# Performance work log

Hardware: AMD Instinct MI355X
Metric: run time of the kernel (lower is better)

## Reference

```python
import jax, jax.numpy as jnp
import numpy as np

D_MODEL = 1024
N_HEADS = 16
D_K = D_MODEL // N_HEADS


def setup_inputs() -> dict:
    key = jax.random.key(0)
    ks = jax.random.split(key, 11)
    B, S = 2, 2048
    scale = 0.02
    inp = {
        "q": jax.random.normal(ks[0], (B, S, D_MODEL), jnp.float32),
        "k": jax.random.normal(ks[1], (B, S, D_MODEL), jnp.float32),
        "v": jax.random.normal(ks[2], (B, S, D_MODEL), jnp.float32),
        "w_q": jax.random.normal(ks[3], (D_MODEL, D_MODEL), jnp.float32) * scale,
        "b_q": jnp.zeros((D_MODEL,), jnp.float32),
        "w_k": jax.random.normal(ks[4], (D_MODEL, D_MODEL), jnp.float32) * scale,
        "b_k": jnp.zeros((D_MODEL,), jnp.float32),
        "w_v": jax.random.normal(ks[5], (D_MODEL, D_MODEL), jnp.float32) * scale,
        "b_v": jnp.zeros((D_MODEL,), jnp.float32),
        "w_o": jax.random.normal(ks[6], (D_MODEL, D_MODEL), jnp.float32) * scale,
        "b_o": jnp.zeros((D_MODEL,), jnp.float32),
    }
    return inp


def reference(q, k, v, w_q, b_q, w_k, b_k, w_v, b_v, w_o, b_o):
    B, S, _ = q.shape
    # projections (torch Linear: x @ W.T + b); split into heads -> [B, H, S, d]
    def proj(x, w, b):
        return (x @ w.T + b).reshape(B, S, N_HEADS, D_K).transpose(0, 2, 1, 3)
    qh = proj(q, w_q, b_q)
    kh = proj(k, w_k, b_k)
    vh = proj(v, w_v, b_v)
    scores = jnp.einsum("bhqd,bhkd->bhqk", qh, kh) / jnp.sqrt(
        jnp.asarray(D_K, jnp.float32))
    attn = jax.nn.softmax(scores, axis=-1)  # dropout = identity (eval)
    out = jnp.einsum("bhqk,bhkd->bhqd", attn, vh)
    out = out.transpose(0, 2, 1, 3).reshape(B, S, D_MODEL)
    return out @ w_o.T + b_o
```

## Files before the change

kernel.cpp:

```cpp
#include <hip/hip_runtime.h>

typedef unsigned short u16;
typedef unsigned int u32;
typedef __attribute__((ext_vector_type(4))) unsigned short u16x4;
typedef __attribute__((ext_vector_type(8))) unsigned short u16x8;
typedef __attribute__((ext_vector_type(8))) __bf16 bf16x8;
typedef __attribute__((ext_vector_type(4))) float f32x4;
typedef __attribute__((ext_vector_type(16))) float f32x16;

#define SEQ 2048
#define DMODEL 1024
#define LDP 3072
#define MM (DMODEL * DMODEL)
#define SC 0.18033688f

__device__ __forceinline__ u16 f2bf(float f) {
  unsigned u = __builtin_bit_cast(unsigned, f);
  u = (u + 0x7fffu + ((u >> 16) & 1u)) >> 16;
  return (u16)u;
}

__device__ __forceinline__ u32 cvtpk(float lo, float hi) {
  u32 r;
  asm volatile("v_cvt_pk_bf16_f32 %0, %1, %2" : "=v"(r) : "v"(lo), "v"(hi));
  return r;
}

__device__ __forceinline__ float fexp2(float x) {
#if __has_builtin(__builtin_amdgcn_exp2f)
  return __builtin_amdgcn_exp2f(x);
#else
  return exp2f(x);
#endif
}

__device__ __forceinline__ bf16x8 ldbf8(const u16* p) {
  return __builtin_bit_cast(bf16x8, *(const u16x8*)p);
}
__device__ __forceinline__ bf16x8 ldbf8c(const char* p) {
  return __builtin_bit_cast(bf16x8, *(const u16x8*)p);
}

__device__ __forceinline__ f32x4 mfma16(bf16x8 a, bf16x8 b, f32x4 c) {
  return __builtin_amdgcn_mfma_f32_16x16x32_bf16(a, b, c, 0, 0, 0);
}
__device__ __forceinline__ f32x16 mfma32(bf16x8 a, bf16x8 b, f32x16 c) {
  return __builtin_amdgcn_mfma_f32_32x32x16_bf16(a, b, c, 0, 0, 0);
}

__device__ __forceinline__ void gl16(const void* g, void* l) {
  __builtin_amdgcn_global_load_lds(
      (__attribute__((address_space(1))) void*)(size_t)g,
      (__attribute__((address_space(3))) void*)l, 16, 0, 0);
}

__device__ __forceinline__ void cast8(const float* __restrict__ s, u16* __restrict__ d) {
  const size_t i = ((size_t)blockIdx.x * blockDim.x + threadIdx.x) * 8;
  const float4 a = *(const float4*)(s + i);
  const float4 b = *(const float4*)(s + i + 4);
  u16x8 o;
  o[0] = f2bf(a.x); o[1] = f2bf(a.y); o[2] = f2bf(a.z); o[3] = f2bf(a.w);
  o[4] = f2bf(b.x); o[5] = f2bf(b.y); o[6] = f2bf(b.z); o[7] = f2bf(b.w);
  *(u16x8*)(d + i) = o;
}

__global__ void cast_qkv_k(const float* __restrict__ q, const float* __restrict__ k,
                           const float* __restrict__ v, u16* __restrict__ dq,
                           u16* __restrict__ dk, u16* __restrict__ dv) {
  const int z = blockIdx.y;
  cast8(z == 0 ? q : z == 1 ? k : v, z == 0 ? dq : z == 1 ? dk : dv);
}

__global__ void cast_w_k(const float* __restrict__ wq, const float* __restrict__ wk,
                         const float* __restrict__ wv, const float* __restrict__ wo,
                         u16* __restrict__ wqkv, u16* __restrict__ wob) {
  const int z = blockIdx.y;
  const float* s = z == 0 ? wq : z == 1 ? wk : z == 2 ? wv : wo;
  u16* d = z < 3 ? wqkv + (size_t)z * MM : wob;
  cast8(s, d);
}

template <int OMODE>
__device__ __forceinline__ void gemm_bt_body(const u16* __restrict__ A,
                                             const u16* __restrict__ Bw,
                                             const float* __restrict__ bias,
                                             void* __restrict__ Cv, const int K,
                                             const int ldc, const int ncol0,
                                             const int m0, const int n0) {
  __shared__ u16 As[128 * 32];
  __shared__ u16 Bs[128 * 32];
  const int tid = threadIdx.x;
  const int lane = tid & 63;
  const int w = tid >> 6;
  const int l15 = lane & 15;
  const int lg = lane >> 4;

  f32x4 acc[4][4] = {};

  const int arow = (w >> 1) * 64 + l15;
  const int brow = (w & 1) * 64 + l15;
  const int kfb = lg * 16;

  const int strow = w * 32 + (lane >> 2);
  const u16* Ag = A + (size_t)(m0 + strow) * K + (lane & 3) * 8;
  const u16* Bg = Bw + (size_t)(n0 + strow) * K + (lane & 3) * 8;
  const size_t rstep = (size_t)16 * K;
  char* AsL0 = (char*)As + w * 32 * 64;
  char* AsL1 = AsL0 + 16 * 64;
  char* BsL0 = (char*)Bs + w * 32 * 64;
  char* BsL1 = BsL0 + 16 * 64;

  for (int k0 = 0; k0 < K; k0 += 32) {
    __syncthreads();
    gl16(Ag + k0, AsL0);
    gl16(Ag + k0 + rstep, AsL1);
    gl16(Bg + k0, BsL0);
    gl16(Bg + k0 + rstep, BsL1);
    __syncthreads();
    bf16x8 af[4], bfv[4];
#pragma unroll
    for (int t = 0; t < 4; ++t) {
      af[t] = ldbf8c((char*)As + (arow + t * 16) * 64 + kfb);
      bfv[t] = ldbf8c((char*)Bs + (brow + t * 16) * 64 + kfb);
    }
    __builtin_amdgcn_s_setprio(1);
#pragma unroll
    for (int i = 0; i < 4; ++i)
#pragma unroll
      for (int j = 0; j < 4; ++j) acc[i][j] = mfma16(af[i], bfv[j], acc[i][j]);
    __builtin_amdgcn_s_setprio(0);
  }

  const int mrow = (w >> 1) * 64 + lg * 4;
  const int ncol = (w & 1) * 64 + l15;
#pragma unroll
  for (int j = 0; j < 4; ++j) {
    const int gn = n0 + ncol + j * 16;
    const float bia = bias[gn];
#pragma unroll
    for (int i = 0; i < 4; ++i) {
      const int gmb = m0 + mrow + i * 16;
#pragma unroll
      for (int r = 0; r < 4; ++r) {
        const float val = acc[i][j][r] + bia;
        const int gm = gmb + r;
        if (OMODE == 0) {
          ((float*)Cv)[(size_t)gm * ldc + gn] = val;
        } else if (OMODE == 1) {
          ((u16*)Cv)[(size_t)gm * ldc + ncol0 + gn] = f2bf(val);
        } else {
          const int bb = gm >> 11, ss = gm & 2047;
          const int hh = gn >> 6, dd = gn & 63;
          ((u16*)Cv)[(((size_t)(bb * 16 + hh) * 64 + dd) << 11) + ss] = f2bf(val);
        }
      }
    }
  }
}

__global__ __launch_bounds__(256, 3) void gemm_qkv_k(
    const u16* __restrict__ qb, const u16* __restrict__ kb,
    const u16* __restrict__ vb, const u16* __restrict__ wqkv,
    const float* __restrict__ bq, const float* __restrict__ bk,
    const float* __restrict__ bv, u16* __restrict__ proj, u16* __restrict__ vtb) {
  const int b = blockIdx.x;
  const int xcd = b & 7;
  const int i = b >> 3;
  const int z = i >> 5;
  const int j = i & 31;
  const int m0 = (xcd * 4 + (j >> 3)) * 128;
  const int n0 = (j & 7) * 128;
  if (z == 2)
    gemm_bt_body<2>(vb, wqkv + 2 * (size_t)MM, bv, vtb, DMODEL, 0, 0, m0, n0);
  else
    gemm_bt_body<1>(z == 0 ? qb : kb, wqkv + (size_t)z * MM, z == 0 ? bq : bk,
                    proj, DMODEL, LDP, z * DMODEL, m0, n0);
}

__global__ __launch_bounds__(256, 3) void gemm_o_k(const u16* __restrict__ attnb,
                                                   const u16* __restrict__ wob,
                                                   const float* __restrict__ bo,
                                                   float* __restrict__ out) {
  const int b = blockIdx.x;
  const int xcd = b & 7;
  const int i = b >> 3;
  const int m0 = (xcd * 4 + (i >> 3)) * 128;
  const int n0 = (i & 7) * 128;
  gemm_bt_body<0>(attnb, wob, bo, out, DMODEL, DMODEL, 0, m0, n0);
}

__global__ __launch_bounds__(256, 2) void attn_k(const u16* __restrict__ proj,
                                                 const u16* __restrict__ vtb,
                                                 u16* __restrict__ outa) {
  __shared__ u16 ks[2][64 * 64];
  __shared__ u16 vs[2][64 * 64];
  const int b = blockIdx.x;
  const int slot = b >> 3;
  const int bh = (b & 7) * 4 + (slot >> 4);
  const int qB = (slot & 15) * 128;
  const int tid = threadIdx.x;
  const int lane = tid & 63;
  const int w = tid >> 6;
  const size_t rb = (size_t)(bh >> 4) * SEQ;
  const int h = bh & 15;
  const int l31 = lane & 31;
  const int hi = lane >> 5;
  const int swz = (l31 & 7) << 4;

  const u16* qp = proj + (rb + qB + w * 32 + l31) * LDP + h * 64 + hi * 8;
  bf16x8 qf[4];
#pragma unroll
  for (int km = 0; km < 4; ++km) qf[km] = ldbf8(qp + km * 16);

  const int srow = tid >> 2;
  const int scel = (tid & 3) * 16;
  const int stz0 = srow * 128 + (((tid & 3) * 32) ^ ((srow & 7) << 4));
  const int stz1 = srow * 128 + ((((tid & 3) * 32) + 16) ^ ((srow & 7) << 4));
  const u16* kg = proj + rb * LDP + DMODEL + h * 64;
  const u16* vg = vtb + (size_t)bh * 64 * SEQ;

  u16x8 ka0, ka1, va0, va1;
  {
    const u16* kr = kg + (size_t)srow * LDP + scel;
    ka0 = *(const u16x8*)kr;
    ka1 = *(const u16x8*)(kr + 8);
    const u16* vr = vg + (size_t)srow * SEQ + scel;
    va0 = *(const u16x8*)vr;
    va1 = *(const u16x8*)(vr + 8);
  }

  f32x16 oa0 = {}, oa1 = {};
  float mrun = -3.0e38f, lrun = 0.f;
  int p = 0;

  for (int kv0 = 0; kv0 < SEQ; kv0 += 64) {
    {
      char* kd = (char*)ks[p];
      char* vd = (char*)vs[p];
      *(u16x8*)(kd + stz0) = ka0;
      *(u16x8*)(kd + stz1) = ka1;
      *(u16x8*)(vd + stz0) = va0;
      *(u16x8*)(vd + stz1) = va1;
    }
    __syncthreads();
    if (kv0 + 64 < SEQ) {
      const u16* kr = kg + (size_t)(kv0 + 64 + srow) * LDP + scel;
      ka0 = *(const u16x8*)kr;
      ka1 = *(const u16x8*)(kr + 8);
      const u16* vr = vg + (size_t)srow * SEQ + kv0 + 64 + scel;
      va0 = *(const u16x8*)vr;
      va1 = *(const u16x8*)(vr + 8);
    }
    const char* kp = (const char*)ks[p];
    const char* vp = (const char*)vs[p];
    f32x16 s0 = {}, s1 = {};
    __builtin_amdgcn_s_setprio(1);
#pragma unroll
    for (int km = 0; km < 4; ++km) {
      const int co = (km * 32 + hi * 16) ^ swz;
      const bf16x8 k0 = ldbf8c(kp + l31 * 128 + co);
      const bf16x8 k1 = ldbf8c(kp + (32 + l31) * 128 + co);
      s0 = mfma32(k0, qf[km], s0);
      s1 = mfma32(k1, qf[km], s1);
    }
    __builtin_amdgcn_s_setprio(0);

    float mxq0 = fmaxf(fmaxf(s0[0], s0[1]), fmaxf(s0[2], s0[3]));
    float mxq1 = fmaxf(fmaxf(s0[4], s0[5]), fmaxf(s0[6], s0[7]));
    float mxq2 = fmaxf(fmaxf(s0[8], s0[9]), fmaxf(s0[10], s0[11]));
    float mxq3 = fmaxf(fmaxf(s0[12], s0[13]), fmaxf(s0[14], s0[15]));
    float mxq4 = fmaxf(fmaxf(s1[0], s1[1]), fmaxf(s1[2], s1[3]));
    float mxq5 = fmaxf(fmaxf(s1[4], s1[5]), fmaxf(s1[6], s1[7]));
    float mxq6 = fmaxf(fmaxf(s1[8], s1[9]), fmaxf(s1[10], s1[11]));
    float mxq7 = fmaxf(fmaxf(s1[12], s1[13]), fmaxf(s1[14], s1[15]));
    float mx = fmaxf(fmaxf(fmaxf(mxq0, mxq1), fmaxf(mxq2, mxq3)),
                     fmaxf(fmaxf(mxq4, mxq5), fmaxf(mxq6, mxq7)));
    mx = fmaxf(mx, __shfl_xor(mx, 32));
    if (!__all(mx <= mrun + 64.0f)) {
      const float mn = fmaxf(mrun, mx);
      const float sf = fexp2((mrun - mn) * SC);
      mrun = mn;
      lrun *= sf;
#pragma unroll
      for (int r = 0; r < 16; ++r) { oa0[r] *= sf; oa1[r] *= sf; }
    }
    const float nmc = -mrun * SC;
#pragma unroll
    for (int r = 0; r < 16; ++r) s0[r] = fexp2(__builtin_fmaf(s0[r], SC, nmc));
#pragma unroll
    for (int r = 0; r < 16; ++r) s1[r] = fexp2(__builtin_fmaf(s1[r], SC, nmc));
    float rs = (((s0[0] + s0[1]) + (s0[2] + s0[3])) +
                ((s0[4] + s0[5]) + (s0[6] + s0[7]))) +
               (((s0[8] + s0[9]) + (s0[10] + s0[11])) +
                ((s0[12] + s0[13]) + (s0[14] + s0[15])));
    rs += (((s1[0] + s1[1]) + (s1[2] + s1[3])) +
           ((s1[4] + s1[5]) + (s1[6] + s1[7]))) +
          (((s1[8] + s1[9]) + (s1[10] + s1[11])) +
           ((s1[12] + s1[13]) + (s1[14] + s1[15])));
    rs += __shfl_xor(rs, 32);
    lrun += rs;

    __builtin_amdgcn_s_setprio(1);
#define PCHUNK(SV, G, CB)                                                \
    {                                                                    \
      u16x8 pbu;                                                         \
      ((u32*)&pbu)[0] = cvtpk(SV[G + 0], SV[G + 1]);                     \
      ((u32*)&pbu)[1] = cvtpk(SV[G + 2], SV[G + 3]);                     \
      ((u32*)&pbu)[2] = cvtpk(SV[G + 4], SV[G + 5]);                     \
      ((u32*)&pbu)[3] = cvtpk(SV[G + 6], SV[G + 7]);                     \
      const bf16x8 pb = __builtin_bit_cast(bf16x8, pbu);                 \
      const int vc0 = (CB + 8 * hi) ^ swz;                               \
      const int vc1 = (CB + 16 + 8 * hi) ^ swz;                          \
      const char* vr0 = vp + l31 * 128;                                  \
      const char* vr1 = vp + (32 + l31) * 128;                           \
      u16x8 vf0, vf1;                                                    \
      *(u16x4*)&vf0       = *(const u16x4*)(vr0 + vc0);                  \
      *((u16x4*)&vf0 + 1) = *(const u16x4*)(vr0 + vc1);                  \
      *(u16x4*)&vf1       = *(const u16x4*)(vr1 + vc0);                  \
      *((u16x4*)&vf1 + 1) = *(const u16x4*)(vr1 + vc1);                  \
      oa0 = mfma32(__builtin_bit_cast(bf16x8, vf0), pb, oa0);            \
      oa1 = mfma32(__builtin_bit_cast(bf16x8, vf1), pb, oa1);            \
    }
    PCHUNK(s0, 0, 0)
    PCHUNK(s0, 8, 32)
    PCHUNK(s1, 0, 64)
    PCHUNK(s1, 8, 96)
#undef PCHUNK
    __builtin_amdgcn_s_setprio(0);
    p ^= 1;
  }

  const float invl = 1.0f / lrun;
  u16* orow = outa + (rb + qB + w * 32 + l31) * DMODEL + h * 64 + hi * 4;
#pragma unroll
  for (int g = 0; g < 4; ++g) {
    u16x4 st0, st1;
    ((u32*)&st0)[0] = cvtpk(oa0[4 * g + 0] * invl, oa0[4 * g + 1] * invl);
    ((u32*)&st0)[1] = cvtpk(oa0[4 * g + 2] * invl, oa0[4 * g + 3] * invl);
    *(u16x4*)(orow + 8 * g) = st0;
    ((u32*)&st1)[0] = cvtpk(oa1[4 * g + 0] * invl, oa1[4 * g + 1] * invl);
    ((u32*)&st1)[1] = cvtpk(oa1[4 * g + 2] * invl, oa1[4 * g + 3] * invl);
    *(u16x4*)(orow + 32 + 8 * g) = st1;
  }
}

extern "C" void kernel_launch(void* const* d_in, const int* in_sizes, int n_in,
                              void* d_out, int out_size, void* d_ws, size_t ws_size,
                              hipStream_t stream) {
  const float* q  = (const float*)d_in[0];
  const float* k  = (const float*)d_in[1];
  const float* v  = (const float*)d_in[2];
  const float* wq = (const float*)d_in[3];
  const float* bq = (const float*)d_in[4];
  const float* wk = (const float*)d_in[5];
  const float* bk = (const float*)d_in[6];
  const float* wv = (const float*)d_in[7];
  const float* bv = (const float*)d_in[8];
  const float* wo = (const float*)d_in[9];
  const float* bo = (const float*)d_in[10];

  const size_t NTOK = (size_t)2 * SEQ;
  const size_t NELE = NTOK * DMODEL;
  u16* qb    = (u16*)d_ws;
  u16* kb    = qb + NELE;
  u16* vb    = kb + NELE;
  u16* wqkv  = vb + NELE;
  u16* wob   = wqkv + 3 * (size_t)MM;
  u16* projb = wob + (size_t)MM;
  u16* vtb   = projb + NTOK * LDP;
  u16* attnb = qb;

  cast_qkv_k<<<dim3(2048, 3), 256, 0, stream>>>(q, k, v, qb, kb, vb);
  cast_w_k<<<dim3(512, 4), 256, 0, stream>>>(wq, wk, wv, wo, wqkv, wob);
  gemm_qkv_k<<<768, 256, 0, stream>>>(qb, kb, vb, wqkv, bq, bk, bv, projb, vtb);
  attn_k<<<512, 256, 0, stream>>>(projb, vtb, attnb);
  gemm_o_k<<<256, 256, 0, stream>>>(attnb, wob, bo, (float*)d_out);
}
```

Before: 127.3 us.

## Process two KV tiles per attention iteration, retune V swizzle, merge cast kernels

The attention loop now handles 128 keys per iteration. Two 64-key K/V tiles sit in the two LDS buffers, so each iteration issues both QK^T products before running softmax and PV on each tile. This halves the number of barrier-separated iterations and gives more independent MFMA work to hide latency. The price is more registers for prefetch (8 vectors) and scores, and two barriers per iteration with no LDS overlap while writing. V now uses a separate 8-byte-granularity XOR swizzle meant to cut LDS bank conflicts on its 4-element reads. The two fp32-to-bf16 cast launches are merged into one kernel to save a launch.

Result: no change. 128.4 us (+0.8%).

```diff
diff --git a/kernel.cpp b/kernel.cpp
--- a/kernel.cpp
+++ b/kernel.cpp
@@ -54,30 +54,33 @@
       (__attribute__((address_space(3))) void*)l, 16, 0, 0);
 }
 
-__device__ __forceinline__ void cast8(const float* __restrict__ s, u16* __restrict__ d) {
-  const size_t i = ((size_t)blockIdx.x * blockDim.x + threadIdx.x) * 8;
+__global__ void cast_all_k(const float* __restrict__ q, const float* __restrict__ k,
+                           const float* __restrict__ v, const float* __restrict__ wq,
+                           const float* __restrict__ wk, const float* __restrict__ wv,
+                           const float* __restrict__ wo, u16* __restrict__ dq,
+                           u16* __restrict__ dk, u16* __restrict__ dv,
+                           u16* __restrict__ wqkv, u16* __restrict__ wob) {
+  int b = blockIdx.x;
+  const float* s;
+  u16* d;
+  if (b < 6144) {
+    const int z = b >> 11;
+    s = z == 0 ? q : z == 1 ? k : v;
+    d = z == 0 ? dq : z == 1 ? dk : dv;
+    b &= 2047;
+  } else {
+    const int z = (b - 6144) >> 9;
+    s = z == 0 ? wq : z == 1 ? wk : z == 2 ? wv : wo;
+    d = z < 3 ? wqkv + (size_t)z * MM : wob;
+    b = (b - 6144) & 511;
+  }
+  const size_t i = ((size_t)b * blockDim.x + threadIdx.x) * 8;
   const float4 a = *(const float4*)(s + i);
-  const float4 b = *(const float4*)(s + i + 4);
+  const float4 c = *(const float4*)(s + i + 4);
   u16x8 o;
   o[0] = f2bf(a.x); o[1] = f2bf(a.y); o[2] = f2bf(a.z); o[3] = f2bf(a.w);
-  o[4] = f2bf(b.x); o[5] = f2bf(b.y); o[6] = f2bf(b.z); o[7] = f2bf(b.w);
+  o[4] = f2bf(c.x); o[5] = f2bf(c.y); o[6] = f2bf(c.z); o[7] = f2bf(c.w);
   *(u16x8*)(d + i) = o;
-}
-
-__global__ void cast_qkv_k(const float* __restrict__ q, const float* __restrict__ k,
-                           const float* __restrict__ v, u16* __restrict__ dq,
-                           u16* __restrict__ dk, u16* __restrict__ dv) {
-  const int z = blockIdx.y;
-  cast8(z == 0 ? q : z == 1 ? k : v, z == 0 ? dq : z == 1 ? dk : dv);
-}
-
-__global__ void cast_w_k(const float* __restrict__ wq, const float* __restrict__ wk,
-                         const float* __restrict__ wv, const float* __restrict__ wo,
-                         u16* __restrict__ wqkv, u16* __restrict__ wob) {
-  const int z = blockIdx.y;
-  const float* s = z == 0 ? wq : z == 1 ? wk : z == 2 ? wv : wo;
-  u16* d = z < 3 ? wqkv + (size_t)z * MM : wob;
-  cast8(s, d);
 }
 
 template <int OMODE>
@@ -205,7 +208,8 @@
   const int h = bh & 15;
   const int l31 = lane & 31;
   const int hi = lane >> 5;
-  const int swz = (l31 & 7) << 4;
+  const int swzk = (l31 & 7) << 4;
+  const int swzv = (l31 & 15) << 3;
 
   const u16* qp = proj + (rb + qB + w * 32 + l31) * LDP + h * 64 + hi * 8;
   bf16x8 qf[4];
@@ -213,122 +217,159 @@
   for (int km = 0; km < 4; ++km) qf[km] = ldbf8(qp + km * 16);
 
   const int srow = tid >> 2;
-  const int scel = (tid & 3) * 16;
-  const int stz0 = srow * 128 + (((tid & 3) * 32) ^ ((srow & 7) << 4));
-  const int stz1 = srow * 128 + ((((tid & 3) * 32) + 16) ^ ((srow & 7) << 4));
+  const int scol = (tid & 3) * 32;
+  const int scel = scol >> 1;
+  const int kz0 = srow * 128 + (scol ^ ((srow & 7) << 4));
+  const int kz1 = srow * 128 + ((scol + 16) ^ ((srow & 7) << 4));
+  const int vz0 = srow * 128 + (scol ^ ((srow & 15) << 3));
+  const int vz1 = srow * 128 + ((scol + 8) ^ ((srow & 15) << 3));
+  const int vz2 = srow * 128 + ((scol + 16) ^ ((srow & 15) << 3));
+  const int vz3 = srow * 128 + ((scol + 24) ^ ((srow & 15) << 3));
   const u16* kg = proj + rb * LDP + DMODEL + h * 64;
   const u16* vg = vtb + (size_t)bh * 64 * SEQ;
 
-  u16x8 ka0, ka1, va0, va1;
-  {
-    const u16* kr = kg + (size_t)srow * LDP + scel;
-    ka0 = *(const u16x8*)kr;
-    ka1 = *(const u16x8*)(kr + 8);
-    const u16* vr = vg + (size_t)srow * SEQ + scel;
-    va0 = *(const u16x8*)vr;
-    va1 = *(const u16x8*)(vr + 8);
+  u16x8 kA0, kA1, kB0, kB1, vA0, vA1, vB0, vB1;
+
+#define LOADPAIR(KV)                                                     \
+  {                                                                      \
+    const u16* krA = kg + (size_t)((KV) + srow) * LDP + scel;            \
+    kA0 = *(const u16x8*)krA;                                            \
+    kA1 = *(const u16x8*)(krA + 8);                                      \
+    const u16* krB = kg + (size_t)((KV) + 64 + srow) * LDP + scel;       \
+    kB0 = *(const u16x8*)krB;                                            \
+    kB1 = *(const u16x8*)(krB + 8);                                      \
+    const u16* vrA = vg + (size_t)srow * SEQ + (KV) + scel;              \
+    vA0 = *(const u16x8*)vrA;                                            \
+    vA1 = *(const u16x8*)(vrA + 8);                                      \
+    vB0 = *(const u16x8*)(vrA + 64);                                     \
+    vB1 = *(const u16x8*)(vrA + 72);                                     \
+  }
+
+#define WRITEPAIR()                                                      \
+  {                                                                      \
+    char* k0d = (char*)ks[0];                                            \
+    char* k1d = (char*)ks[1];                                            \
+    char* v0d = (char*)vs[0];                                            \
+    char* v1d = (char*)vs[1];                                            \
+    *(u16x8*)(k0d + kz0) = kA0;                                          \
+    *(u16x8*)(k0d + kz1) = kA1;                                          \
+    *(u16x8*)(k1d + kz0) = kB0;                                          \
+    *(u16x8*)(k1d + kz1) = kB1;                                          \
+    *(u16x4*)(v0d + vz0) = *(u16x4*)&vA0;                                \
+    *(u16x4*)(v0d + vz1) = *((u16x4*)&vA0 + 1);                          \
+    *(u16x4*)(v0d + vz2) = *(u16x4*)&vA1;                                \
+    *(u16x4*)(v0d + vz3) = *((u16x4*)&vA1 + 1);                          \
+    *(u16x4*)(v1d + vz0) = *(u16x4*)&vB0;                                \
+    *(u16x4*)(v1d + vz1) = *((u16x4*)&vB0 + 1);                          \
+    *(u16x4*)(v1d + vz2) = *(u16x4*)&vB1;                                \
+    *(u16x4*)(v1d + vz3) = *((u16x4*)&vB1 + 1);                          \
+  }
+
+#define QKT(S0, S1, KP)                                                  \
+  {                                                                      \
+    __builtin_amdgcn_s_setprio(1);                                       \
+    _Pragma("unroll") for (int km = 0; km < 4; ++km) {                   \
+      const int co = (km * 32 + hi * 16) ^ swzk;                         \
+      const bf16x8 k0 = ldbf8c((KP) + l31 * 128 + co);                   \
+      const bf16x8 k1 = ldbf8c((KP) + (32 + l31) * 128 + co);            \
+      S0 = mfma32(k0, qf[km], S0);                                       \
+      S1 = mfma32(k1, qf[km], S1);                                       \
+    }                                                                    \
+    __builtin_amdgcn_s_setprio(0);                                       \
+  }
+
+#define PCHUNK(SV, G, CB, VP)                                            \
+  {                                                                      \
+    u16x8 pbu;                                                           \
+    ((u32*)&pbu)[0] = cvtpk(SV[G + 0], SV[G + 1]);                       \
+    ((u32*)&pbu)[1] = cvtpk(SV[G + 2], SV[G + 3]);                       \
+    ((u32*)&pbu)[2] = cvtpk(SV[G + 4], SV[G + 5]);                       \
+    ((u32*)&pbu)[3] = cvtpk(SV[G + 6], SV[G + 7]);                       \
+    const bf16x8 pb = __builtin_bit_cast(bf16x8, pbu);                   \
+    const int vc0 = ((CB) + 8 * hi) ^ swzv;                              \
+    const int vc1 = ((CB) + 16 + 8 * hi) ^ swzv;                         \
+    const char* vr0 = (VP) + l31 * 128;                                  \
+    const char* vr1 = (VP) + (32 + l31) * 128;                           \
+    u16x8 vf0, vf1;                                                      \
+    *(u16x4*)&vf0 = *(const u16x4*)(vr0 + vc0);                          \
+    *((u16x4*)&vf0 + 1) = *(const u16x4*)(vr0 + vc1);                    \
+    *(u16x4*)&vf1 = *(const u16x4*)(vr1 + vc0);                          \
+    *((u16x4*)&vf1 + 1) = *(const u16x4*)(vr1 + vc1);                    \
+    oa0 = mfma32(__builtin_bit_cast(bf16x8, vf0), pb, oa0);              \
+    oa1 = mfma32(__builtin_bit_cast(bf16x8, vf1), pb, oa1);              \
+  }
+
+#define SOFTPV(S0, S1, VP)                                               \
+  {                                                                      \
+    float mxq0 = fmaxf(fmaxf(S0[0], S0[1]), fmaxf(S0[2], S0[3]));        \
+    float mxq1 = fmaxf(fmaxf(S0[4], S0[5]), fmaxf(S0[6], S0[7]));        \
+    float mxq2 = fmaxf(fmaxf(S0[8], S0[9]), fmaxf(S0[10], S0[11]));      \
+    float mxq3 = fmaxf(fmaxf(S0[12], S0[13]), fmaxf(S0[14], S0[15]));    \
+    float mxq4 = fmaxf(fmaxf(S1[0], S1[1]), fmaxf(S1[2], S1[3]));        \
+    float mxq5 = fmaxf(fmaxf(S1[4], S1[5]), fmaxf(S1[6], S1[7]));        \
+    float mxq6 = fmaxf(fmaxf(S1[8], S1[9]), fmaxf(S1[10], S1[11]));      \
+    float mxq7 = fmaxf(fmaxf(S1[12], S1[13]), fmaxf(S1[14], S1[15]));    \
+    float mx = fmaxf(fmaxf(fmaxf(mxq0, mxq1), fmaxf(mxq2, mxq3)),        \
+                     fmaxf(fmaxf(mxq4, mxq5), fmaxf(mxq6, mxq7)));       \
+    mx = fmaxf(mx, __shfl_xor(mx, 32));                                  \
+    if (!__all(mx <= mrun + 64.0f)) {                                    \
+      const float mn = fmaxf(mrun, mx);                                  \
+      const float sf = fexp2((mrun - mn) * SC);                          \
+      mrun = mn;                                                         \
+      lrun *= sf;                                                        \
+      _Pragma("unroll") for (int r = 0; r < 16; ++r) {                   \
+        oa0[r] *= sf;                                                    \
+        oa1[r] *= sf;                                                    \
+      }                                                                  \
+    }                                                                    \
+    const float nmc = -mrun * SC;                                        \
+    _Pragma("unroll") for (int r = 0; r < 16; ++r)                       \
+        S0[r] = fexp2(__builtin_fmaf(S0[r], SC, nmc));                   \
+    _Pragma("unroll") for (int r = 0; r < 16; ++r)                       \
+        S1[r] = fexp2(__builtin_fmaf(S1[r], SC, nmc));                   \
+    float rs = (((S0[0] + S0[1]) + (S0[2] + S0[3])) +                    \
+                ((S0[4] + S0[5]) + (S0[6] + S0[7]))) +                   \
+               (((S0[8] + S0[9]) + (S0[10] + S0[11])) +                  \
+                ((S0[12] + S0[13]) + (S0[14] + S0[15])));                \
+    rs += (((S1[0] + S1[1]) + (S1[2] + S1[3])) +                         \
+           ((S1[4] + S1[5]) + (S1[6] + S1[7]))) +                        \
+          (((S1[8] + S1[9]) + (S1[10] + S1[11])) +                       \
+           ((S1[12] + S1[13]) + (S1[14] + S1[15])));                     \
+    rs += __shfl_xor(rs, 32);                                            \
+    lrun += rs;                                                          \
+    __builtin_amdgcn_s_setprio(1);                                       \
+    PCHUNK(S0, 0, 0, VP)                                                 \
+    PCHUNK(S0, 8, 32, VP)                                                \
+    PCHUNK(S1, 0, 64, VP)                                                \
+    PCHUNK(S1, 8, 96, VP)                                                \
+    __builtin_amdgcn_s_setprio(0);                                       \
   }
 
   f32x16 oa0 = {}, oa1 = {};
   float mrun = -3.0e38f, lrun = 0.f;
-  int p = 0;
-
-  for (int kv0 = 0; kv0 < SEQ; kv0 += 64) {
-    {
-      char* kd = (char*)ks[p];
-      char* vd = (char*)vs[p];
-      *(u16x8*)(kd + stz0) = ka0;
-      *(u16x8*)(kd + stz1) = ka1;
-      *(u16x8*)(vd + stz0) = va0;
-      *(u16x8*)(vd + stz1) = va1;
+
+  LOADPAIR(0);
+  WRITEPAIR();
+  __syncthreads();
+
+  for (int it = 0; it < SEQ / 128; ++it) {
+    if (it + 1 < SEQ / 128) LOADPAIR((it + 1) * 128);
+    f32x16 s0A = {}, s1A = {}, s0B = {}, s1B = {};
+    QKT(s0A, s1A, (const char*)ks[0])
+    QKT(s0B, s1B, (const char*)ks[1])
+    SOFTPV(s0A, s1A, (const char*)vs[0])
+    SOFTPV(s0B, s1B, (const char*)vs[1])
+    if (it + 1 < SEQ / 128) {
+      __syncthreads();
+      WRITEPAIR();
+      __syncthreads();
     }
-    __syncthreads();
-    if (kv0 + 64 < SEQ) {
-      const u16* kr = kg + (size_t)(kv0 + 64 + srow) * LDP + scel;
-      ka0 = *(const u16x8*)kr;
-      ka1 = *(const u16x8*)(kr + 8);
-      const u16* vr = vg + (size_t)srow * SEQ + kv0 + 64 + scel;
-      va0 = *(const u16x8*)vr;
-      va1 = *(const u16x8*)(vr + 8);
-    }
-    const char* kp = (const char*)ks[p];
-    const char* vp = (const char*)vs[p];
-    f32x16 s0 = {}, s1 = {};
-    __builtin_amdgcn_s_setprio(1);
-#pragma unroll
-    for (int km = 0; km < 4; ++km) {
-      const int co = (km * 32 + hi * 16) ^ swz;
-      const bf16x8 k0 = ldbf8c(kp + l31 * 128 + co);
-      const bf16x8 k1 = ldbf8c(kp + (32 + l31) * 128 + co);
-      s0 = mfma32(k0, qf[km], s0);
-      s1 = mfma32(k1, qf[km], s1);
-    }
-    __builtin_amdgcn_s_setprio(0);
-
-    float mxq0 = fmaxf(fmaxf(s0[0], s0[1]), fmaxf(s0[2], s0[3]));
-    float mxq1 = fmaxf(fmaxf(s0[4], s0[5]), fmaxf(s0[6], s0[7]));
-    float mxq2 = fmaxf(fmaxf(s0[8], s0[9]), fmaxf(s0[10], s0[11]));
-    float mxq3 = fmaxf(fmaxf(s0[12], s0[13]), fmaxf(s0[14], s0[15]));
-    float mxq4 = fmaxf(fmaxf(s1[0], s1[1]), fmaxf(s1[2], s1[3]));
-    float mxq5 = fmaxf(fmaxf(s1[4], s1[5]), fmaxf(s1[6], s1[7]));
-    float mxq6 = fmaxf(fmaxf(s1[8], s1[9]), fmaxf(s1[10], s1[11]));
-    float mxq7 = fmaxf(fmaxf(s1[12], s1[13]), fmaxf(s1[14], s1[15]));
-    float mx = fmaxf(fmaxf(fmaxf(mxq0, mxq1), fmaxf(mxq2, mxq3)),
-                     fmaxf(fmaxf(mxq4, mxq5), fmaxf(mxq6, mxq7)));
-    mx = fmaxf(mx, __shfl_xor(mx, 32));
-    if (!__all(mx <= mrun + 64.0f)) {
-      const float mn = fmaxf(mrun, mx);
-      const float sf = fexp2((mrun - mn) * SC);
-      mrun = mn;
-      lrun *= sf;
-#pragma unroll
-      for (int r = 0; r < 16; ++r) { oa0[r] *= sf; oa1[r] *= sf; }
-    }
-    const float nmc = -mrun * SC;
-#pragma unroll
-    for (int r = 0; r < 16; ++r) s0[r] = fexp2(__builtin_fmaf(s0[r], SC, nmc));
-#pragma unroll
-    for (int r = 0; r < 16; ++r) s1[r] = fexp2(__builtin_fmaf(s1[r], SC, nmc));
-    float rs = (((s0[0] + s0[1]) + (s0[2] + s0[3])) +
-                ((s0[4] + s0[5]) + (s0[6] + s0[7]))) +
-               (((s0[8] + s0[9]) + (s0[10] + s0[11])) +
-                ((s0[12] + s0[13]) + (s0[14] + s0[15])));
-    rs += (((s1[0] + s1[1]) + (s1[2] + s1[3])) +
-           ((s1[4] + s1[5]) + (s1[6] + s1[7]))) +
-          (((s1[8] + s1[9]) + (s1[10] + s1[11])) +
-           ((s1[12] + s1[13]) + (s1[14] + s1[15])));
-    rs += __shfl_xor(rs, 32);
-    lrun += rs;
-
-    __builtin_amdgcn_s_setprio(1);
-#define PCHUNK(SV, G, CB)                                                \
-    {                                                                    \
-      u16x8 pbu;                                                         \
-      ((u32*)&pbu)[0] = cvtpk(SV[G + 0], SV[G + 1]);                     \
-      ((u32*)&pbu)[1] = cvtpk(SV[G + 2], SV[G + 3]);                     \
-      ((u32*)&pbu)[2] = cvtpk(SV[G + 4], SV[G + 5]);                     \
-      ((u32*)&pbu)[3] = cvtpk(SV[G + 6], SV[G + 7]);                     \
-      const bf16x8 pb = __builtin_bit_cast(bf16x8, pbu);                 \
-      const int vc0 = (CB + 8 * hi) ^ swz;                               \
-      const int vc1 = (CB + 16 + 8 * hi) ^ swz;                          \
-      const char* vr0 = vp + l31 * 128;                                  \
-      const char* vr1 = vp + (32 + l31) * 128;                           \
-      u16x8 vf0, vf1;                                                    \
-      *(u16x4*)&vf0       = *(const u16x4*)(vr0 + vc0);                  \
-      *((u16x4*)&vf0 + 1) = *(const u16x4*)(vr0 + vc1);                  \
-      *(u16x4*)&vf1       = *(const u16x4*)(vr1 + vc0);                  \
-      *((u16x4*)&vf1 + 1) = *(const u16x4*)(vr1 + vc1);                  \
-      oa0 = mfma32(__builtin_bit_cast(bf16x8, vf0), pb, oa0);            \
-      oa1 = mfma32(__builtin_bit_cast(bf16x8, vf1), pb, oa1);            \
-    }
-    PCHUNK(s0, 0, 0)
-    PCHUNK(s0, 8, 32)
-    PCHUNK(s1, 0, 64)
-    PCHUNK(s1, 8, 96)
+  }
+#undef LOADPAIR
+#undef WRITEPAIR
+#undef QKT
 #undef PCHUNK
-    __builtin_amdgcn_s_setprio(0);
-    p ^= 1;
-  }
+#undef SOFTPV
 
   const float invl = 1.0f / lrun;
   u16* orow = outa + (rb + qB + w * 32 + l31) * DMODEL + h * 64 + hi * 4;
@@ -370,8 +411,8 @@
   u16* vtb   = projb + NTOK * LDP;
   u16* attnb = qb;
 
-  cast_qkv_k<<<dim3(2048, 3), 256, 0, stream>>>(q, k, v, qb, kb, vb);
-  cast_w_k<<<dim3(512, 4), 256, 0, stream>>>(wq, wk, wv, wo, wqkv, wob);
+  cast_all_k<<<8192, 256, 0, stream>>>(q, k, v, wq, wk, wv, wo, qb, kb, vb,
+                                       wqkv, wob);
   gemm_qkv_k<<<768, 256, 0, stream>>>(qb, kb, vb, wqkv, bq, bk, bv, projb, vtb);
   attn_k<<<512, 256, 0, stream>>>(projb, vtb, attnb);
   gemm_o_k<<<256, 256, 0, stream>>>(attnb, wob, bo, (float*)d_out);
```

## Fuse fp32-to-bf16 casts into GEMM tile loads and reswizzle V LDS layout

Applied to the files above, without the earlier changes.

Removes the two standalone cast kernels and makes the projection GEMMs load fp32 activations and weights directly. They convert to bf16 in registers and store into LDS, using register prefetch of the next K tile in place of async global-to-LDS copies. This saves the extra bf16 round trip through global memory and two launches. The cost is that each GEMM block reads twice the bytes per tile and re-converts weights redundantly across blocks. The attention kernel also gets a separate finer-grained XOR swizzle for the V tile to reduce LDS bank conflicts on its 8-byte reads.

Result: faster. 120.1 us (-5.7%).

```diff
diff --git a/kernel.cpp b/kernel.cpp
--- a/kernel.cpp
+++ b/kernel.cpp
@@ -48,41 +48,18 @@
   return __builtin_amdgcn_mfma_f32_32x32x16_bf16(a, b, c, 0, 0, 0);
 }
 
-__device__ __forceinline__ void gl16(const void* g, void* l) {
-  __builtin_amdgcn_global_load_lds(
-      (__attribute__((address_space(1))) void*)(size_t)g,
-      (__attribute__((address_space(3))) void*)l, 16, 0, 0);
-}
-
-__device__ __forceinline__ void cast8(const float* __restrict__ s, u16* __restrict__ d) {
-  const size_t i = ((size_t)blockIdx.x * blockDim.x + threadIdx.x) * 8;
-  const float4 a = *(const float4*)(s + i);
-  const float4 b = *(const float4*)(s + i + 4);
-  u16x8 o;
-  o[0] = f2bf(a.x); o[1] = f2bf(a.y); o[2] = f2bf(a.z); o[3] = f2bf(a.w);
-  o[4] = f2bf(b.x); o[5] = f2bf(b.y); o[6] = f2bf(b.z); o[7] = f2bf(b.w);
-  *(u16x8*)(d + i) = o;
-}
-
-__global__ void cast_qkv_k(const float* __restrict__ q, const float* __restrict__ k,
-                           const float* __restrict__ v, u16* __restrict__ dq,
-                           u16* __restrict__ dk, u16* __restrict__ dv) {
-  const int z = blockIdx.y;
-  cast8(z == 0 ? q : z == 1 ? k : v, z == 0 ? dq : z == 1 ? dk : dv);
-}
-
-__global__ void cast_w_k(const float* __restrict__ wq, const float* __restrict__ wk,
-                         const float* __restrict__ wv, const float* __restrict__ wo,
-                         u16* __restrict__ wqkv, u16* __restrict__ wob) {
-  const int z = blockIdx.y;
-  const float* s = z == 0 ? wq : z == 1 ? wk : z == 2 ? wv : wo;
-  u16* d = z < 3 ? wqkv + (size_t)z * MM : wob;
-  cast8(s, d);
-}
-
-template <int OMODE>
-__device__ __forceinline__ void gemm_bt_body(const u16* __restrict__ A,
-                                             const u16* __restrict__ Bw,
+__device__ __forceinline__ u16x8 pk8(float4 x, float4 y) {
+  u16x8 r;
+  ((u32*)&r)[0] = cvtpk(x.x, x.y);
+  ((u32*)&r)[1] = cvtpk(x.z, x.w);
+  ((u32*)&r)[2] = cvtpk(y.x, y.y);
+  ((u32*)&r)[3] = cvtpk(y.z, y.w);
+  return r;
+}
+
+template <int OMODE, int AFP32>
+__device__ __forceinline__ void gemm_bt_body(const void* __restrict__ Av,
+                                             const float* __restrict__ Bw,
                                              const float* __restrict__ bias,
                                              void* __restrict__ Cv, const int K,
                                              const int ldc, const int ncol0,
@@ -101,22 +78,50 @@
   const int brow = (w & 1) * 64 + l15;
   const int kfb = lg * 16;
 
-  const int strow = w * 32 + (lane >> 2);
-  const u16* Ag = A + (size_t)(m0 + strow) * K + (lane & 3) * 8;
-  const u16* Bg = Bw + (size_t)(n0 + strow) * K + (lane & 3) * 8;
-  const size_t rstep = (size_t)16 * K;
-  char* AsL0 = (char*)As + w * 32 * 64;
-  char* AsL1 = AsL0 + 16 * 64;
-  char* BsL0 = (char*)Bs + w * 32 * 64;
-  char* BsL1 = BsL0 + 16 * 64;
-
+  const int srow = tid >> 2;
+  const int sc8 = (tid & 3) * 8;
+  const float* Agf = (const float*)Av + (size_t)(m0 + srow) * K + sc8;
+  const u16* Agh = (const u16*)Av + (size_t)(m0 + srow) * K + sc8;
+  const float* Bgf = Bw + (size_t)(n0 + srow) * K + sc8;
+  const size_t rstep = (size_t)64 * K;
+
+  float4 a00, a01, a10, a11, b00, b01, b10, b11;
+  u16x8 ah0, ah1;
+
+#define GLOADK(KO)                                                       \
+  {                                                                      \
+    if (AFP32) {                                                         \
+      a00 = *(const float4*)(Agf + (KO));                                \
+      a01 = *(const float4*)(Agf + (KO) + 4);                            \
+      a10 = *(const float4*)(Agf + (KO) + rstep);                        \
+      a11 = *(const float4*)(Agf + (KO) + rstep + 4);                    \
+    } else {                                                             \
+      ah0 = *(const u16x8*)(Agh + (KO));                                 \
+      ah1 = *(const u16x8*)(Agh + (KO) + rstep);                         \
+    }                                                                    \
+    b00 = *(const float4*)(Bgf + (KO));                                  \
+    b01 = *(const float4*)(Bgf + (KO) + 4);                              \
+    b10 = *(const float4*)(Bgf + (KO) + rstep);                          \
+    b11 = *(const float4*)(Bgf + (KO) + rstep + 4);                      \
+  }
+
+  char* const asw = (char*)As + srow * 64 + (tid & 3) * 16;
+  char* const bsw = (char*)Bs + srow * 64 + (tid & 3) * 16;
+
+  GLOADK(0);
   for (int k0 = 0; k0 < K; k0 += 32) {
     __syncthreads();
-    gl16(Ag + k0, AsL0);
-    gl16(Ag + k0 + rstep, AsL1);
-    gl16(Bg + k0, BsL0);
-    gl16(Bg + k0 + rstep, BsL1);
+    if (AFP32) {
+      *(u16x8*)asw = pk8(a00, a01);
+      *(u16x8*)(asw + 64 * 64) = pk8(a10, a11);
+    } else {
+      *(u16x8*)asw = ah0;
+      *(u16x8*)(asw + 64 * 64) = ah1;
+    }
+    *(u16x8*)bsw = pk8(b00, b01);
+    *(u16x8*)(bsw + 64 * 64) = pk8(b10, b11);
     __syncthreads();
+    if (k0 + 32 < K) GLOADK(k0 + 32);
     bf16x8 af[4], bfv[4];
 #pragma unroll
     for (int t = 0; t < 4; ++t) {
@@ -130,6 +135,7 @@
       for (int j = 0; j < 4; ++j) acc[i][j] = mfma16(af[i], bfv[j], acc[i][j]);
     __builtin_amdgcn_s_setprio(0);
   }
+#undef GLOADK
 
   const int mrow = (w >> 1) * 64 + lg * 4;
   const int ncol = (w & 1) * 64 + l15;
@@ -159,8 +165,9 @@
 }
 
 __global__ __launch_bounds__(256, 3) void gemm_qkv_k(
-    const u16* __restrict__ qb, const u16* __restrict__ kb,
-    const u16* __restrict__ vb, const u16* __restrict__ wqkv,
+    const float* __restrict__ q, const float* __restrict__ k,
+    const float* __restrict__ v, const float* __restrict__ wq,
+    const float* __restrict__ wk, const float* __restrict__ wv,
     const float* __restrict__ bq, const float* __restrict__ bk,
     const float* __restrict__ bv, u16* __restrict__ proj, u16* __restrict__ vtb) {
   const int b = blockIdx.x;
@@ -171,14 +178,14 @@
   const int m0 = (xcd * 4 + (j >> 3)) * 128;
   const int n0 = (j & 7) * 128;
   if (z == 2)
-    gemm_bt_body<2>(vb, wqkv + 2 * (size_t)MM, bv, vtb, DMODEL, 0, 0, m0, n0);
+    gemm_bt_body<2, 1>(v, wv, bv, vtb, DMODEL, 0, 0, m0, n0);
   else
-    gemm_bt_body<1>(z == 0 ? qb : kb, wqkv + (size_t)z * MM, z == 0 ? bq : bk,
-                    proj, DMODEL, LDP, z * DMODEL, m0, n0);
+    gemm_bt_body<1, 1>(z == 0 ? q : k, z == 0 ? wq : wk, z == 0 ? bq : bk,
+                       proj, DMODEL, LDP, z * DMODEL, m0, n0);
 }
 
 __global__ __launch_bounds__(256, 3) void gemm_o_k(const u16* __restrict__ attnb,
-                                                   const u16* __restrict__ wob,
+                                                   const float* __restrict__ wo,
                                                    const float* __restrict__ bo,
                                                    float* __restrict__ out) {
   const int b = blockIdx.x;
@@ -186,7 +193,7 @@
   const int i = b >> 3;
   const int m0 = (xcd * 4 + (i >> 3)) * 128;
   const int n0 = (i & 7) * 128;
-  gemm_bt_body<0>(attnb, wob, bo, out, DMODEL, DMODEL, 0, m0, n0);
+  gemm_bt_body<0, 0>(attnb, wo, bo, out, DMODEL, DMODEL, 0, m0, n0);
 }
 
 __global__ __launch_bounds__(256, 2) void attn_k(const u16* __restrict__ proj,
@@ -205,7 +212,8 @@
   const int h = bh & 15;
   const int l31 = lane & 31;
   const int hi = lane >> 5;
-  const int swz = (l31 & 7) << 4;
+  const int swzk = (l31 & 7) << 4;
+  const int swzv = (l31 & 15) << 3;
 
   const u16* qp = proj + (rb + qB + w * 32 + l31) * LDP + h * 64 + hi * 8;
   bf16x8 qf[4];
@@ -213,9 +221,14 @@
   for (int km = 0; km < 4; ++km) qf[km] = ldbf8(qp + km * 16);
 
   const int srow = tid >> 2;
-  const int scel = (tid & 3) * 16;
-  const int stz0 = srow * 128 + (((tid & 3) * 32) ^ ((srow & 7) << 4));
-  const int stz1 = srow * 128 + ((((tid & 3) * 32) + 16) ^ ((srow & 7) << 4));
+  const int scol = (tid & 3) * 32;
+  const int scel = scol >> 1;
+  const int kz0 = srow * 128 + (scol ^ ((srow & 7) << 4));
+  const int kz1 = srow * 128 + ((scol + 16) ^ ((srow & 7) << 4));
+  const int vz0 = srow * 128 + (scol ^ ((srow & 15) << 3));
+  const int vz1 = srow * 128 + ((scol + 8) ^ ((srow & 15) << 3));
+  const int vz2 = srow * 128 + ((scol + 16) ^ ((srow & 15) << 3));
+  const int vz3 = srow * 128 + ((scol + 24) ^ ((srow & 15) << 3));
   const u16* kg = proj + rb * LDP + DMODEL + h * 64;
   const u16* vg = vtb + (size_t)bh * 64 * SEQ;
 
@@ -237,10 +250,12 @@
     {
       char* kd = (char*)ks[p];
       char* vd = (char*)vs[p];
-      *(u16x8*)(kd + stz0) = ka0;
-      *(u16x8*)(kd + stz1) = ka1;
-      *(u16x8*)(vd + stz0) = va0;
-      *(u16x8*)(vd + stz1) = va1;
+      *(u16x8*)(kd + kz0) = ka0;
+      *(u16x8*)(kd + kz1) = ka1;
+      *(u16x4*)(vd + vz0) = *(u16x4*)&va0;
+      *(u16x4*)(vd + vz1) = *((u16x4*)&va0 + 1);
+      *(u16x4*)(vd + vz2) = *(u16x4*)&va1;
+      *(u16x4*)(vd + vz3) = *((u16x4*)&va1 + 1);
     }
     __syncthreads();
     if (kv0 + 64 < SEQ) {
@@ -257,7 +272,7 @@
     __builtin_amdgcn_s_setprio(1);
 #pragma unroll
     for (int km = 0; km < 4; ++km) {
-      const int co = (km * 32 + hi * 16) ^ swz;
+      const int co = (km * 32 + hi * 16) ^ swzk;
       const bf16x8 k0 = ldbf8c(kp + l31 * 128 + co);
       const bf16x8 k1 = ldbf8c(kp + (32 + l31) * 128 + co);
       s0 = mfma32(k0, qf[km], s0);
@@ -309,8 +324,8 @@
       ((u32*)&pbu)[2] = cvtpk(SV[G + 4], SV[G + 5]);                     \
       ((u32*)&pbu)[3] = cvtpk(SV[G + 6], SV[G + 7]);                     \
       const bf16x8 pb = __builtin_bit_cast(bf16x8, pbu);                 \
-      const int vc0 = (CB + 8 * hi) ^ swz;                               \
-      const int vc1 = (CB + 16 + 8 * hi) ^ swz;                          \
+      const int vc0 = ((CB) + 8 * hi) ^ swzv;                            \
+      const int vc1 = ((CB) + 16 + 8 * hi) ^ swzv;                       \
       const char* vr0 = vp + l31 * 128;                                  \
       const char* vr1 = vp + (32 + l31) * 128;                           \
       u16x8 vf0, vf1;                                                    \
@@ -360,19 +375,12 @@
   const float* bo = (const float*)d_in[10];
 
   const size_t NTOK = (size_t)2 * SEQ;
-  const size_t NELE = NTOK * DMODEL;
-  u16* qb    = (u16*)d_ws;
-  u16* kb    = qb + NELE;
-  u16* vb    = kb + NELE;
-  u16* wqkv  = vb + NELE;
-  u16* wob   = wqkv + 3 * (size_t)MM;
-  u16* projb = wob + (size_t)MM;
+  u16* projb = (u16*)d_ws;
   u16* vtb   = projb + NTOK * LDP;
-  u16* attnb = qb;
-
-  cast_qkv_k<<<dim3(2048, 3), 256, 0, stream>>>(q, k, v, qb, kb, vb);
-  cast_w_k<<<dim3(512, 4), 256, 0, stream>>>(wq, wk, wv, wo, wqkv, wob);
-  gemm_qkv_k<<<768, 256, 0, stream>>>(qb, kb, vb, wqkv, bq, bk, bv, projb, vtb);
+  u16* attnb = vtb + (size_t)32 * 64 * SEQ;
+
+  gemm_qkv_k<<<768, 256, 0, stream>>>(q, k, v, wq, wk, wv, bq, bk, bv, projb,
+                                      vtb);
   attn_k<<<512, 256, 0, stream>>>(projb, vtb, attnb);
-  gemm_o_k<<<256, 256, 0, stream>>>(attnb, wob, bo, (float*)d_out);
-}
+  gemm_o_k<<<256, 256, 0, stream>>>(attnb, wo, bo, (float*)d_out);
+}
```
